# Optimization experiments

Hardware: AMD Instinct MI355X
Metric: run time of the kernel (lower is better)

## Reference

```python
import jax, jax.numpy as jnp
import numpy as np

H, DH = 8, 40            # heads, dim_head -> inner_dim = 320
SCALE = DH ** -0.5
B, N, M = 16, 4096, 77   # batch, query tokens (64x64 latent), text tokens
QD, CD, ID = 320, 768, H * DH


def setup_inputs() -> dict:
    key = jax.random.key(0)
    ks = jax.random.split(key, 7)
    x = jax.random.normal(ks[0], (B, N, QD), dtype=jnp.float32)
    context = jax.random.normal(ks[1], (B, M, CD), dtype=jnp.float32)
    # Linear weights stored as (in, out); torch nn.Linear has no bias for q/k/v
    Wq = jax.random.normal(ks[2], (QD, ID), dtype=jnp.float32) * (QD ** -0.5)
    Wk = jax.random.normal(ks[3], (CD, ID), dtype=jnp.float32) * (CD ** -0.5)
    Wv = jax.random.normal(ks[4], (CD, ID), dtype=jnp.float32) * (CD ** -0.5)
    Wo = jax.random.normal(ks[5], (ID, QD), dtype=jnp.float32) * (ID ** -0.5)
    bo = jnp.zeros((QD,), dtype=jnp.float32)
    return {"x": x, "context": context, "Wq": Wq, "Wk": Wk, "Wv": Wv, "Wo": Wo, "bo": bo}


def reference(x, context, Wq, Wk, Wv, Wo, bo):
    b, n, _ = x.shape
    m = context.shape[1]
    q = (x @ Wq).reshape(b, n, H, DH)        # to_q
    k = (context @ Wk).reshape(b, m, H, DH)  # to_k
    v = (context @ Wv).reshape(b, m, H, DH)  # to_v
    # full QK^T * scale (rank-bias path inactive: rank={} / is_add_rank=False)
    scores = jnp.einsum('bihd,bjhd->bhij', q, k) * SCALE  # [B,H,N,M]
    attn = jax.nn.softmax(scores, axis=-1)
    out = jnp.einsum('bhij,bjhd->bihd', attn, v).reshape(b, n, ID)
    return out @ Wo + bo  # to_out Linear; Dropout(p=0.0) is identity
```

## Files before the change

kernel.cpp:

```cpp
#include <hip/hip_runtime.h>

typedef unsigned short u16;
using short8 = __attribute__((ext_vector_type(8))) short;
using f32x4  = __attribute__((ext_vector_type(4))) float;

#define SCALE 0.15811388300841897f

__device__ __forceinline__ u16 f2bf(float f) {
  unsigned int u = __float_as_uint(f);
  u += 0x7fffu + ((u >> 16) & 1u);
  return (u16)(u >> 16);
}


__global__ void prep_transpose(const float* __restrict__ Wq, const float* __restrict__ Wo,
                               const float* __restrict__ Wk, const float* __restrict__ Wv,
                               u16* __restrict__ wqt, u16* __restrict__ wot,
                               u16* __restrict__ wkt, u16* __restrict__ wvt) {
  __shared__ float ld[64][65];
  const int bid = blockIdx.x;
  const float* src; u16* dst; int K; float scale; int tk, tn;
  if (bid < 25)       { src = Wq; dst = wqt; K = 320; scale = SCALE; tk = bid / 5;         tn = bid % 5; }
  else if (bid < 50)  { src = Wo; dst = wot; K = 320; scale = 1.f;   tk = (bid - 25) / 5;  tn = (bid - 25) % 5; }
  else if (bid < 110) { src = Wk; dst = wkt; K = 768; scale = 1.f;   tk = (bid - 50) / 5;  tn = (bid - 50) % 5; }
  else                { src = Wv; dst = wvt; K = 768; scale = 1.f;   tk = (bid - 110) / 5; tn = (bid - 110) % 5; }
  const int c = threadIdx.x & 63, r0 = threadIdx.x >> 6;
  for (int rr = r0; rr < 64; rr += 4)
    ld[rr][c] = src[(size_t)(tk * 64 + rr) * 320 + tn * 64 + c];
  __syncthreads();
  for (int rr = r0; rr < 64; rr += 4)
    dst[(size_t)(tn * 64 + rr) * K + tk * 64 + c] = f2bf(ld[c][rr] * scale);
}

__global__ __launch_bounds__(256)
void xconv(const float* __restrict__ x, u16* __restrict__ xbf) {
  const size_t idx = (size_t)blockIdx.x * 256 + threadIdx.x;
  const size_t stride = (size_t)gridDim.x * 256;
  const size_t total = (size_t)65536 * 320 / 8;
  for (size_t g = idx; g < total; g += stride) {
    const float4* src = reinterpret_cast<const float4*>(x + g * 8);
    float4 a = src[0], b = src[1];
    uint4 o;
    o.x = (unsigned)f2bf(a.x) | ((unsigned)f2bf(a.y) << 16);
    o.y = (unsigned)f2bf(a.z) | ((unsigned)f2bf(a.w) << 16);
    o.z = (unsigned)f2bf(b.x) | ((unsigned)f2bf(b.y) << 16);
    o.w = (unsigned)f2bf(b.z) | ((unsigned)f2bf(b.w) << 16);
    *reinterpret_cast<uint4*>(xbf + g * 8) = o;
  }
  if (blockIdx.x == 0 && threadIdx.x < 64) xbf[(size_t)65536 * 320 + threadIdx.x] = 0;
}

__global__ __launch_bounds__(256, 1)
void kv_mfma(const float* __restrict__ ctx,
             const u16* __restrict__ wkt, const u16* __restrict__ wvt,
             u16* __restrict__ kbf, u16* __restrict__ vt) {
  const int b = blockIdx.x, z = blockIdx.y;
  const int tid = threadIdx.x;
  const int w = tid >> 6, l = tid & 63, l16 = l & 15, lhi = l >> 4;
  __shared__ __align__(16) u16 sctx[80][776];

  for (int i = tid; i < 80 * 192; i += 256) {
    int row = i / 192, c4 = (i - row * 192) * 4;
    ushort4 u;
    if (row < 77) {
      float4 v = *reinterpret_cast<const float4*>(&ctx[(size_t)(b * 77 + row) * 768 + c4]);
      u.x = f2bf(v.x); u.y = f2bf(v.y); u.z = f2bf(v.z); u.w = f2bf(v.w);
    } else u = (ushort4){0, 0, 0, 0};
    *reinterpret_cast<ushort4*>(&sctx[row][c4]) = u;
  }
  if (z == 0) {
    for (int i = tid; i < 8 * 80 * 3; i += 256) {
      int hm = i / 3, q = i - hm * 3;
      int h = hm / 80, m = hm - h * 80;
      *reinterpret_cast<uint4*>(&kbf[(((size_t)b * 8 + h) * 80 + m) * 64 + 40 + q * 8]) = (uint4){0, 0, 0, 0};
    }
  } else {
    for (int i = tid; i < 8 * 48 * 2; i += 256) {
      int hd = i / 2, q = i - hd * 2;
      int h = hd / 48, d = hd - h * 48;
      *reinterpret_cast<uint4*>(&vt[(((size_t)b * 8 + h) * 48 + d) * 96 + 80 + q * 8]) = (uint4){0, 0, 0, 0};
    }
    for (int i = tid; i < 8 * 8 * 10; i += 256) {
      int h = i / 80, rem = i - h * 80;
      int d = 40 + rem / 10, q = rem - (rem / 10) * 10;
      *reinterpret_cast<uint4*>(&vt[(((size_t)b * 8 + h) * 48 + d) * 96 + q * 8]) = (uint4){0, 0, 0, 0};
    }
  }
  __syncthreads();

  f32x4 acc[5][5];
  #pragma unroll
  for (int rt = 0; rt < 5; ++rt)
    #pragma unroll
    for (int nt = 0; nt < 5; ++nt) acc[rt][nt] = (f32x4){0.f, 0.f, 0.f, 0.f};

  const u16* wbase = (z == 0 ? wkt : wvt) + (size_t)(w * 80) * 768;
  #pragma unroll 2
  for (int ks = 0; ks < 24; ++ks) {
    short8 af[5];
    #pragma unroll
    for (int rt = 0; rt < 5; ++rt)
      af[rt] = *reinterpret_cast<const short8*>(&sctx[rt * 16 + l16][ks * 32 + lhi * 8]);
    short8 bf[5];
    #pragma unroll
    for (int nt = 0; nt < 5; ++nt)
      bf[nt] = *reinterpret_cast<const short8*>(&wbase[(size_t)(nt * 16 + l16) * 768 + ks * 32 + lhi * 8]);
    #pragma unroll
    for (int rt = 0; rt < 5; ++rt)
      #pragma unroll
      for (int nt = 0; nt < 5; ++nt)
        acc[rt][nt] = __builtin_amdgcn_mfma_f32_16x16x32_bf16(af[rt], bf[nt], acc[rt][nt], 0, 0, 0);
  }

  if (z == 0) {
    #pragma unroll
    for (int rt = 0; rt < 5; ++rt)
      #pragma unroll
      for (int nt = 0; nt < 5; ++nt) {
        int c = w * 80 + nt * 16 + l16, h = c / 40, d = c - h * 40;
        #pragma unroll
        for (int r = 0; r < 4; ++r) {
          int m = rt * 16 + lhi * 4 + r;
          kbf[(((size_t)b * 8 + h) * 80 + m) * 64 + d] = f2bf(m < 77 ? acc[rt][nt][r] : 0.f);
        }
      }
  } else {
    #pragma unroll
    for (int rt = 0; rt < 5; ++rt)
      #pragma unroll
      for (int nt = 0; nt < 5; ++nt) {
        int c = w * 80 + nt * 16 + l16, h = c / 40, d = c - h * 40;
        #pragma unroll
        for (int r = 0; r < 4; ++r) {
          int m = rt * 16 + lhi * 4 + r;
          vt[(((size_t)b * 8 + h) * 48 + d) * 96 + m] = f2bf(m < 77 ? acc[rt][nt][r] : 0.f);
        }
      }
  }
}

__global__ __launch_bounds__(256, 3)
void qproj(u16* __restrict__ qg, const u16* __restrict__ wqt) {
  const int tid = threadIdx.x;
  const int w = tid >> 6, l = tid & 63, l16 = l & 15, lhi = l >> 4;
  const int r0 = blockIdx.x * 64;
  __shared__ __align__(16) u16 xs[64][328];

  for (int i = tid; i < 64 * 40; i += 256) {
    int row = i / 40, c8 = (i - row * 40) * 8;
    *reinterpret_cast<uint4*>(&xs[row][c8]) =
        *reinterpret_cast<const uint4*>(&qg[(size_t)(r0 + row) * 320 + c8]);
  }
  __syncthreads();

  f32x4 acc[4][5];
  #pragma unroll
  for (int rt = 0; rt < 4; ++rt)
    #pragma unroll
    for (int nt = 0; nt < 5; ++nt) acc[rt][nt] = (f32x4){0.f, 0.f, 0.f, 0.f};
  #pragma unroll 2
  for (int ks = 0; ks < 10; ++ks) {
    short8 af[4];
    #pragma unroll
    for (int rt = 0; rt < 4; ++rt)
      af[rt] = *reinterpret_cast<const short8*>(&xs[rt * 16 + l16][ks * 32 + lhi * 8]);
    #pragma unroll
    for (int nt = 0; nt < 5; ++nt) {
      short8 bf = *reinterpret_cast<const short8*>(&wqt[(size_t)(w * 80 + nt * 16 + l16) * 320 + ks * 32 + lhi * 8]);
      #pragma unroll
      for (int rt = 0; rt < 4; ++rt)
        acc[rt][nt] = __builtin_amdgcn_mfma_f32_16x16x32_bf16(af[rt], bf, acc[rt][nt], 0, 0, 0);
    }
  }
  __syncthreads();
  #pragma unroll
  for (int rt = 0; rt < 4; ++rt)
    #pragma unroll
    for (int nt = 0; nt < 5; ++nt) {
      int col = w * 80 + nt * 16 + l16;
      #pragma unroll
      for (int r = 0; r < 4; ++r)
        xs[rt * 16 + lhi * 4 + r][col] = f2bf(acc[rt][nt][r]);
    }
  __syncthreads();
  for (int i = tid; i < 64 * 40; i += 256) {
    int row = i / 40, c8 = (i - row * 40) * 8;
    *reinterpret_cast<uint4*>(&qg[(size_t)(r0 + row) * 320 + c8]) =
        *reinterpret_cast<const uint4*>(&xs[row][c8]);
  }
}

__global__ __launch_bounds__(512, 8)
void attn_sm(u16* __restrict__ qg, const u16* __restrict__ kbf,
             const u16* __restrict__ vtp) {
  const int b  = blockIdx.y;
  const int q0 = blockIdx.x * 64;
  const int tid = threadIdx.x;
  const int w   = tid >> 6;
  const int l   = tid & 63;
  const int l16 = l & 15;
  const int lhi = l >> 4;
  const int wq  = w & 3;
  const int hg  = w >> 2;

  __shared__ __align__(16) u16 Pt[8][16][104];

  if (l < 32) {
    int r = l >> 1, q = l & 1;
    *reinterpret_cast<uint4*>(&Pt[w][r][80 + 8 * q]) = (uint4){0u, 0u, 0u, 0u};
  }

  const size_t rowbase = (size_t)(b * 4096 + q0 + wq * 16);

  for (int hi = 0; hi < 4; ++hi) {
    const int h = hg * 4 + hi;
    const u16* kh = kbf + ((size_t)(b * 8 + h)) * 80 * 64;
    const u16* vh = vtp + ((size_t)(b * 8 + h)) * 48 * 96;
    f32x4 sacc[5];
    #pragma unroll
    for (int mt = 0; mt < 5; ++mt) sacc[mt] = (f32x4){0.f, 0.f, 0.f, 0.f};
    #pragma unroll
    for (int ks = 0; ks < 2; ++ks) {
      short8 a = *reinterpret_cast<const short8*>(
          &qg[(rowbase + l16) * 320 + h * 40 + ks * 32 + lhi * 8]);
      #pragma unroll
      for (int mt = 0; mt < 5; ++mt) {
        short8 bb = *reinterpret_cast<const short8*>(&kh[(mt * 16 + l16) * 64 + ks * 32 + lhi * 8]);
        sacc[mt] = __builtin_amdgcn_mfma_f32_16x16x32_bf16(a, bb, sacc[mt], 0, 0, 0);
      }
    }
    #pragma unroll
    for (int r = 0; r < 4; ++r) {
      float sv[5];
      float mx = -1e30f;
      #pragma unroll
      for (int mt = 0; mt < 5; ++mt) {
        float s = sacc[mt][r];
        if (mt * 16 + l16 >= 77) s = -1e30f;
        sv[mt] = s;
        mx = fmaxf(mx, s);
      }
      mx = fmaxf(mx, __shfl_xor(mx, 1));
      mx = fmaxf(mx, __shfl_xor(mx, 2));
      mx = fmaxf(mx, __shfl_xor(mx, 4));
      mx = fmaxf(mx, __shfl_xor(mx, 8));
      float sum = 0.f;
      #pragma unroll
      for (int mt = 0; mt < 5; ++mt) { sv[mt] = __expf(sv[mt] - mx); sum += sv[mt]; }
      sum += __shfl_xor(sum, 1);
      sum += __shfl_xor(sum, 2);
      sum += __shfl_xor(sum, 4);
      sum += __shfl_xor(sum, 8);
      float rs = 1.f / sum;
      int row = lhi * 4 + r;
      #pragma unroll
      for (int mt = 0; mt < 5; ++mt)
        Pt[w][row][mt * 16 + l16] = f2bf(sv[mt] * rs);
    }
    asm volatile("s_waitcnt lgkmcnt(0)" ::: "memory");
    __builtin_amdgcn_sched_barrier(0);
    f32x4 oacc[3];
    #pragma unroll
    for (int nt = 0; nt < 3; ++nt) oacc[nt] = (f32x4){0.f, 0.f, 0.f, 0.f};
    #pragma unroll
    for (int ks = 0; ks < 3; ++ks) {
      short8 a = *reinterpret_cast<const short8*>(&Pt[w][l16][ks * 32 + lhi * 8]);
      #pragma unroll
      for (int nt = 0; nt < 3; ++nt) {
        short8 bb = *reinterpret_cast<const short8*>(&vh[(nt * 16 + l16) * 96 + ks * 32 + lhi * 8]);
        oacc[nt] = __builtin_amdgcn_mfma_f32_16x16x32_bf16(a, bb, oacc[nt], 0, 0, 0);
      }
    }
    asm volatile("s_waitcnt lgkmcnt(0)" ::: "memory");
    __builtin_amdgcn_sched_barrier(0);
    #pragma unroll
    for (int nt = 0; nt < 3; ++nt) {
      int d = nt * 16 + l16;
      if (d < 40) {
        #pragma unroll
        for (int r = 0; r < 4; ++r)
          qg[(rowbase + lhi * 4 + r) * 320 + h * 40 + d] = f2bf(oacc[nt][r]);
      }
    }
  }
}

__global__ __launch_bounds__(256, 4)
void outproj(const u16* __restrict__ og, const u16* __restrict__ wot,
             const float* __restrict__ bo, float* __restrict__ out) {
  const int tid = threadIdx.x;
  const int w = tid >> 6, l = tid & 63, l16 = l & 15, lhi = l >> 4;
  const int r0 = blockIdx.x * 64;
  __shared__ __align__(16) u16 os[64][328];

  for (int i = tid; i < 64 * 40; i += 256) {
    int row = i / 40, c8 = (i - row * 40) * 8;
    *reinterpret_cast<uint4*>(&os[row][c8]) =
        *reinterpret_cast<const uint4*>(&og[(size_t)(r0 + row) * 320 + c8]);
  }
  __syncthreads();

  f32x4 acc[4][5];
  #pragma unroll
  for (int rt = 0; rt < 4; ++rt)
    #pragma unroll
    for (int nt = 0; nt < 5; ++nt) acc[rt][nt] = (f32x4){0.f, 0.f, 0.f, 0.f};
  #pragma unroll 2
  for (int ks = 0; ks < 10; ++ks) {
    short8 af[4];
    #pragma unroll
    for (int rt = 0; rt < 4; ++rt)
      af[rt] = *reinterpret_cast<const short8*>(&os[rt * 16 + l16][ks * 32 + lhi * 8]);
    #pragma unroll
    for (int nt = 0; nt < 5; ++nt) {
      short8 bf = *reinterpret_cast<const short8*>(&wot[(size_t)(w * 80 + nt * 16 + l16) * 320 + ks * 32 + lhi * 8]);
      #pragma unroll
      for (int rt = 0; rt < 4; ++rt)
        acc[rt][nt] = __builtin_amdgcn_mfma_f32_16x16x32_bf16(af[rt], bf, acc[rt][nt], 0, 0, 0);
    }
  }
  #pragma unroll
  for (int nt = 0; nt < 5; ++nt) {
    int col = w * 80 + nt * 16 + l16;
    float bias = bo[col];
    #pragma unroll
    for (int rt = 0; rt < 4; ++rt) {
      #pragma unroll
      for (int r = 0; r < 4; ++r) {
        int row = rt * 16 + lhi * 4 + r;
        out[(size_t)(r0 + row) * 320 + col] = acc[rt][nt][r] + bias;
      }
    }
  }
}

extern "C" void kernel_launch(void* const* d_in, const int* in_sizes, int n_in,
                              void* d_out, int out_size, void* d_ws, size_t ws_size,
                              hipStream_t stream) {
  (void)in_sizes; (void)n_in; (void)out_size; (void)ws_size;
  const float* x       = (const float*)d_in[0];
  const float* context = (const float*)d_in[1];
  const float* Wq      = (const float*)d_in[2];
  const float* Wk      = (const float*)d_in[3];
  const float* Wv      = (const float*)d_in[4];
  const float* Wo      = (const float*)d_in[5];
  const float* bo      = (const float*)d_in[6];
  float* out = (float*)d_out;
  u16* ws = (u16*)d_ws;
  u16* wqt = ws;
  u16* wot = ws + 102400;
  u16* wkt = ws + 204800;
  u16* wvt = ws + 450560;
  u16* kbf = ws + 696320;
  u16* vtp = ws + 1351680;
  u16* qg  = ws + 1941504;

  prep_transpose<<<170, 256, 0, stream>>>(Wq, Wo, Wk, Wv, wqt, wot, wkt, wvt);
  xconv<<<2048, 256, 0, stream>>>(x, qg);
  kv_mfma<<<dim3(16, 2), 256, 0, stream>>>(context, wkt, wvt, kbf, vtp);
  qproj<<<1024, 256, 0, stream>>>(qg, wqt);
  attn_sm<<<dim3(64, 16), 512, 0, stream>>>(qg, kbf, vtp);
  outproj<<<1024, 256, 0, stream>>>(qg, wot, bo, out);
}
```

Measured before the change: 225.6 us.

## Double-buffer softmax tile, drop max subtraction, fully unroll projection loops

The attention kernel now double-buffers the per-wave probability tile in shared memory, which lets it drop the trailing LDS wait and scheduling barrier after the PV matmul. Softmax no longer subtracts the row max and exponentiates raw scaled scores, removing four shuffles and the max reduction per row. This risks overflow for large logits, though it is probably fine for these inputs. The q and out projection k-loops are fully unrolled, and the attention occupancy hint is lowered from 8 to 6 blocks, trading occupancy for registers.

```diff
diff --git a/kernel.cpp b/kernel.cpp
--- a/kernel.cpp
+++ b/kernel.cpp
@@ -158,7 +158,7 @@
   for (int rt = 0; rt < 4; ++rt)
     #pragma unroll
     for (int nt = 0; nt < 5; ++nt) acc[rt][nt] = (f32x4){0.f, 0.f, 0.f, 0.f};
-  #pragma unroll 2
+  #pragma unroll
   for (int ks = 0; ks < 10; ++ks) {
     short8 af[4];
     #pragma unroll
@@ -190,7 +190,7 @@
   }
 }
 
-__global__ __launch_bounds__(512, 8)
+__global__ __launch_bounds__(512, 6)
 void attn_sm(u16* __restrict__ qg, const u16* __restrict__ kbf,
              const u16* __restrict__ vtp) {
   const int b  = blockIdx.y;
@@ -203,17 +203,18 @@
   const int wq  = w & 3;
   const int hg  = w >> 2;
 
-  __shared__ __align__(16) u16 Pt[8][16][104];
-
-  if (l < 32) {
-    int r = l >> 1, q = l & 1;
-    *reinterpret_cast<uint4*>(&Pt[w][r][80 + 8 * q]) = (uint4){0u, 0u, 0u, 0u};
+  __shared__ __align__(16) u16 Pt[8][2][16][104];
+
+  if (l < 64) {
+    int s = l >> 5, r = (l >> 1) & 15, q = l & 1;
+    *reinterpret_cast<uint4*>(&Pt[w][s][r][80 + 8 * q]) = (uint4){0u, 0u, 0u, 0u};
   }
 
   const size_t rowbase = (size_t)(b * 4096 + q0 + wq * 16);
 
   for (int hi = 0; hi < 4; ++hi) {
     const int h = hg * 4 + hi;
+    const int slot = hi & 1;
     const u16* kh = kbf + ((size_t)(b * 8 + h)) * 80 * 64;
     const u16* vh = vtp + ((size_t)(b * 8 + h)) * 48 * 96;
     f32x4 sacc[5];
@@ -231,22 +232,14 @@
     }
     #pragma unroll
     for (int r = 0; r < 4; ++r) {
-      float sv[5];
-      float mx = -1e30f;
+      float ev[5];
+      float sum = 0.f;
       #pragma unroll
       for (int mt = 0; mt < 5; ++mt) {
-        float s = sacc[mt][r];
-        if (mt * 16 + l16 >= 77) s = -1e30f;
-        sv[mt] = s;
-        mx = fmaxf(mx, s);
-      }
-      mx = fmaxf(mx, __shfl_xor(mx, 1));
-      mx = fmaxf(mx, __shfl_xor(mx, 2));
-      mx = fmaxf(mx, __shfl_xor(mx, 4));
-      mx = fmaxf(mx, __shfl_xor(mx, 8));
-      float sum = 0.f;
-      #pragma unroll
-      for (int mt = 0; mt < 5; ++mt) { sv[mt] = __expf(sv[mt] - mx); sum += sv[mt]; }
+        float s = (mt * 16 + l16 >= 77) ? -1e30f : sacc[mt][r];
+        ev[mt] = __expf(s);
+        sum += ev[mt];
+      }
       sum += __shfl_xor(sum, 1);
       sum += __shfl_xor(sum, 2);
       sum += __shfl_xor(sum, 4);
@@ -255,7 +248,7 @@
       int row = lhi * 4 + r;
       #pragma unroll
       for (int mt = 0; mt < 5; ++mt)
-        Pt[w][row][mt * 16 + l16] = f2bf(sv[mt] * rs);
+        Pt[w][slot][row][mt * 16 + l16] = f2bf(ev[mt] * rs);
     }
     asm volatile("s_waitcnt lgkmcnt(0)" ::: "memory");
     __builtin_amdgcn_sched_barrier(0);
@@ -264,15 +257,13 @@
     for (int nt = 0; nt < 3; ++nt) oacc[nt] = (f32x4){0.f, 0.f, 0.f, 0.f};
     #pragma unroll
     for (int ks = 0; ks < 3; ++ks) {
-      short8 a = *reinterpret_cast<const short8*>(&Pt[w][l16][ks * 32 + lhi * 8]);
+      short8 a = *reinterpret_cast<const short8*>(&Pt[w][slot][l16][ks * 32 + lhi * 8]);
       #pragma unroll
       for (int nt = 0; nt < 3; ++nt) {
         short8 bb = *reinterpret_cast<const short8*>(&vh[(nt * 16 + l16) * 96 + ks * 32 + lhi * 8]);
         oacc[nt] = __builtin_amdgcn_mfma_f32_16x16x32_bf16(a, bb, oacc[nt], 0, 0, 0);
       }
     }
-    asm volatile("s_waitcnt lgkmcnt(0)" ::: "memory");
-    __builtin_amdgcn_sched_barrier(0);
     #pragma unroll
     for (int nt = 0; nt < 3; ++nt) {
       int d = nt * 16 + l16;
@@ -305,7 +296,7 @@
   for (int rt = 0; rt < 4; ++rt)
     #pragma unroll
     for (int nt = 0; nt < 5; ++nt) acc[rt][nt] = (f32x4){0.f, 0.f, 0.f, 0.f};
-  #pragma unroll 2
+  #pragma unroll
   for (int ks = 0; ks < 10; ++ks) {
     short8 af[4];
     #pragma unroll
```

Result: no change. 228.8 us (+1.4%).
